# Kernel optimization log

Measured on AMD Instinct MI355X. Metric: run time of the kernel, lower is better.

Reference implementation:

```python
import jax, jax.numpy as jnp
import numpy as np

N_NODES = 10000
N_EDGES = 160000
C = 128           # channel multiplicity
D_DOWN = 64       # node_feats_down '64x0e'
D_RAD = 8         # radial basis size
AVG_NEIGH = 16.0
INV_SQRT3 = 1.0 / np.sqrt(3.0)  # CG coeff for 1o x 1o -> 0e


def setup_inputs() -> dict:
    key = jax.random.key(0)
    ks = jax.random.split(key, 20)
    inp = {
        "node_attrs": jax.random.normal(ks[0], (N_NODES, 10), jnp.float32),
        "node_feats": jax.random.normal(ks[1], (N_NODES, 4 * C), jnp.float32),
        "edge_attrs": jax.random.normal(ks[2], (N_EDGES, 4), jnp.float32),
        "edge_feats": jax.random.uniform(ks[3], (N_EDGES, D_RAD), jnp.float32),
        "edge_index": jax.random.randint(ks[4], (N_EDGES, 2), 0, N_NODES, jnp.int32),
        # linear_up: 128x0e+128x1o -> 128x0e+128x1o (per-irrep channel mixing)
        "W_up0": jax.random.normal(ks[5], (C, C), jnp.float32),
        "W_up1": jax.random.normal(ks[6], (C, C), jnp.float32),
        # linear_down: 128x0e+128x1o -> 64x0e (only scalars map)
        "W_down": jax.random.normal(ks[7], (C, D_DOWN), jnp.float32),
        # radial MLP [136, 256, 256, 256, 512]
        "Wm0": jax.random.normal(ks[8], (D_RAD + 2 * D_DOWN, 256), jnp.float32),
        "Wm1": jax.random.normal(ks[9], (256, 256), jnp.float32),
        "Wm2": jax.random.normal(ks[10], (256, 256), jnp.float32),
        "Wm3": jax.random.normal(ks[11], (256, 4 * C), jnp.float32),
        # linear: irreps_mid (2x128x0e + 2x128x1o) -> 128x0e+128x1o
        "W_lin0": jax.random.normal(ks[12], (2 * C, C), jnp.float32),
        "W_lin1": jax.random.normal(ks[13], (2 * C, C), jnp.float32),
        # skip_linear: 128x0e+128x1o -> 128x0e+128x1o
        "W_skip0": jax.random.normal(ks[14], (C, C), jnp.float32),
        "W_skip1": jax.random.normal(ks[15], (C, C), jnp.float32),
    }
    return inp


def _split(x):
    # [N, 512] -> scalars [N,128], vectors [N,128,3]
    return x[:, :C], x[:, C:].reshape(-1, C, 3)


def _irrep_linear(s, v, W0, W1):
    # e3nn Linear with 1/sqrt(fan_in) normalization, per-irrep
    a = (s @ W0) / np.sqrt(C)
    b = jnp.einsum("nic,ij->njc", v, W1) / np.sqrt(C)
    return a, b


def reference(node_attrs, node_feats, edge_attrs, edge_feats, edge_index,
              W_up0, W_up1, W_down, Wm0, Wm1, Wm2, Wm3,
              W_lin0, W_lin1, W_skip0, W_skip1):
    n_nodes = node_feats.shape[0]
    sender = edge_index[:, 0]
    receiver = edge_index[:, 1]

    s, v = _split(node_feats)

    # skip connection
    sc_s, sc_v = _irrep_linear(s, v, W_skip0, W_skip1)
    sc = jnp.concatenate([sc_s, sc_v.reshape(n_nodes, 3 * C)], axis=-1)

    # linear_up / linear_down
    up_s, up_v = _irrep_linear(s, v, W_up0, W_up1)
    down = (s @ W_down) / np.sqrt(C)  # [N, 64]

    # radial MLP on augmented edge feats
    aug = jnp.concatenate([edge_feats, down[sender], down[receiver]], axis=-1)  # [E,136]
    h = jax.nn.silu((aug @ Wm0) / np.sqrt(aug.shape[-1]))
    h = jax.nn.silu((h @ Wm1) / np.sqrt(256.0))
    h = jax.nn.silu((h @ Wm2) / np.sqrt(256.0))
    tpw = (h @ Wm3) / np.sqrt(256.0)  # [E, 512]
    w1, w2, w3, w4 = tpw[:, :C], tpw[:, C:2*C], tpw[:, 2*C:3*C], tpw[:, 3*C:]

    # per-edge CG tensor product (uvu, external weights)
    xs = up_s[sender]           # [E,128] gathered 0e
    xv = up_v[sender]           # [E,128,3] gathered 1o
    y0 = edge_attrs[:, :1]      # [E,1]   sh 0e
    yv = edge_attrs[:, 1:4]     # [E,3]   sh 1o

    out0a = w1 * xs * y0                                       # 0e x 0e -> 0e
    out0b = w4 * jnp.einsum("eic,ec->ei", xv, yv) * INV_SQRT3  # 1o x 1o -> 0e
    out1a = (w2 * xs)[:, :, None] * yv[:, None, :]             # 0e x 1o -> 1o
    out1b = w3[:, :, None] * xv * y0[:, :, None]               # 1o x 0e -> 1o

    mid0 = jnp.concatenate([out0a, out0b], axis=-1)  # [E,256]
    mid1 = jnp.concatenate([out1a, out1b], axis=1)   # [E,256,3]

    # scatter-sum messages to receivers
    m0 = jax.ops.segment_sum(mid0, receiver, num_segments=n_nodes)
    m1 = jax.ops.segment_sum(mid1, receiver, num_segments=n_nodes)

    # final per-irrep linear, divided by avg_num_neighbors
    msg_s = (m0 @ W_lin0) / np.sqrt(2.0 * C) / AVG_NEIGH                       # [N,128]
    msg_v = jnp.einsum("nic,ij->njc", m1, W_lin1) / np.sqrt(2.0 * C) / AVG_NEIGH  # [N,128,3]

    # reshape_irreps: [N, channels, 1+3]
    out = jnp.concatenate([msg_s[:, :, None], msg_v], axis=-1)  # [N,128,4]
    return out, sc
```

## Files before the change

### kernel.cpp

```cpp
#include <hip/hip_runtime.h>
#include <cmath>

#define NN 10000
#define NE 160000
#define INV_SQRT_C 0.08838834764831845f
#define INV_SQRT3F 0.5773502691896258f

typedef _Float16 f16x8 __attribute__((ext_vector_type(8)));
typedef _Float16 f16x4 __attribute__((ext_vector_type(4)));
typedef _Float16 f16x2 __attribute__((ext_vector_type(2)));
typedef float    f32x4 __attribute__((ext_vector_type(4)));

__device__ __forceinline__ float silu_f(float x) {
  return x / (1.f + __expf(-x));
}

__device__ __forceinline__ void wconv_one(
    int bx, const float* __restrict__ src, _Float16* __restrict__ dst,
    int Korig, int Kpad, int N, float scale, int P) {
  int total = Kpad * N;
  for (int t = bx * 256 + threadIdx.x; t < total; t += 128 * 256) {
    int n = t % N;
    int k = t / N;
    int kb = k >> 5, kk = k & 31;
    int sub = n & (P - 1);
    int n_l = (n & ~(P - 1)) | ((sub & 15) * (P >> 4) + (sub >> 4));
    float v = (k < Korig) ? src[(size_t)k * N + n_l] * scale : 0.f;
    dst[((size_t)(kb * N + n) << 5) + kk] = (_Float16)v;
  }
}

__device__ __forceinline__ void wconv_pair(
    int bx, const float* __restrict__ A, const float* __restrict__ B,
    _Float16* __restrict__ dst, float scale) {
  int tgl = bx * 256 + threadIdx.x;
  int n = tgl & 255;
  int k = tgl >> 8;
  int kb = k >> 5, kk = k & 31;
  int sub = n & 63;
  int n_l = (n & ~63) | ((sub & 15) * 4 + (sub >> 4));
  float v = ((n_l < 128) ? A[(size_t)k * 128 + n_l]
                         : B[(size_t)k * 128 + (n_l - 128)]) * scale;
  dst[((size_t)(kb * 256 + n) << 5) + kk] = (_Float16)v;
}

__device__ __forceinline__ void wconv_dn(
    int bx, const float* __restrict__ src, _Float16* __restrict__ dst,
    float scale) {
  int tgl = bx * 256 + threadIdx.x;
  int n = tgl & 63;
  int k = tgl >> 6;
  int kb = k >> 5, kk = k & 31;
  float v = src[(size_t)k * 64 + n] * scale;
  dst[((size_t)(kb * 64 + n) << 5) + kk] = (_Float16)v;
}

__global__ __launch_bounds__(256) void wconv9(
    const float* __restrict__ s0, const float* __restrict__ s1,
    const float* __restrict__ s2, const float* __restrict__ s3,
    const float* __restrict__ s4, const float* __restrict__ s5,
    _Float16* __restrict__ d0, _Float16* __restrict__ d1,
    _Float16* __restrict__ d2, _Float16* __restrict__ d3,
    _Float16* __restrict__ d4, _Float16* __restrict__ d5,
    const float* __restrict__ W_up0, const float* __restrict__ W_skip0,
    const float* __restrict__ W_up1, const float* __restrict__ W_skip1,
    const float* __restrict__ W_down,
    _Float16* __restrict__ WS0h, _Float16* __restrict__ WS1h,
    _Float16* __restrict__ WDh,
    const int* __restrict__ edge_index,
    int* __restrict__ CNT, int* __restrict__ CNT2) {
  const int b = blockIdx.x;
  if (b < 768) {
    const int job = b >> 7, bx = b & 127;
    switch (job) {
      case 0: wconv_one(bx, s0, d0, 136, 160, 256, 0.08574929257125442f, 64); break;
      case 1: wconv_one(bx, s1, d1, 256, 256, 256, 0.0625f, 64); break;
      case 2: wconv_one(bx, s2, d2, 256, 256, 256, 0.0625f, 64); break;
      case 3: wconv_one(bx, s3, d3, 256, 256, 512, 0.0625f, 32); break;
      case 4: wconv_one(bx, s4, d4, 256, 256, 128, 1.0f / 256.0f, 32); break;
      default: wconv_one(bx, s5, d5, 256, 256, 128, 1.0f / 256.0f, 32); break;
    }
  } else if (b < 896) {
    wconv_pair(b - 768, W_up0, W_skip0, WS0h, INV_SQRT_C);
  } else if (b < 1024) {
    wconv_pair(b - 896, W_up1, W_skip1, WS1h, INV_SQRT_C);
  } else if (b < 1056) {
    wconv_dn(b - 1024, W_down, WDh, INV_SQRT_C);
  } else {
    int e = (b - 1056) * 256 + threadIdx.x;
    if (e < NE) {
      int2 sr = *(const int2*)&edge_index[(size_t)e * 2];
      atomicAdd(&CNT[sr.y], 1);
      atomicAdd(&CNT2[sr.x], 1);
    }
  }
}

__global__ __launch_bounds__(256) void prep2(
    const float* __restrict__ feats,
    const _Float16* __restrict__ WS0h, const _Float16* __restrict__ WS1h,
    const _Float16* __restrict__ WDh,
    _Float16* __restrict__ UPH, _Float16* __restrict__ DOWNH,
    float* __restrict__ out_sc) {
  __shared__ _Float16 As[64 * 128];
  const int b = blockIdx.x;
  const int t = threadIdx.x;
  const int lane = t & 63;
  const int wv = t >> 6;
  const int m = lane & 15;
  const int g = lane >> 4;
  f32x4 zero4 = {0.f, 0.f, 0.f, 0.f};
  f16x8 zf = {0, 0, 0, 0, 0, 0, 0, 0};

  if (b < 157) {
    const int n0 = b * 64;
    for (int idx = t; idx < 1024; idx += 256) {
      int r = idx >> 4, c8 = idx & 15;
      int n = n0 + r;
      f16x8 av = zf;
      if (n < NN) {
        const float* src = &feats[(size_t)n * 512 + c8 * 8];
        float4 f0 = *(const float4*)src;
        float4 f1 = *(const float4*)(src + 4);
        av[0] = (_Float16)f0.x; av[1] = (_Float16)f0.y;
        av[2] = (_Float16)f0.z; av[3] = (_Float16)f0.w;
        av[4] = (_Float16)f1.x; av[5] = (_Float16)f1.y;
        av[6] = (_Float16)f1.z; av[7] = (_Float16)f1.w;
      }
      int sb = (c8 >> 1) ^ (r & 7);
      *(f16x8*)&As[r * 128 + (sb << 4) + (c8 & 1) * 8] = av;
    }
    __syncthreads();

    f32x4 acc[4][4];
    f32x4 acc2[4];
#pragma unroll
    for (int rt = 0; rt < 4; ++rt) {
      acc2[rt] = zero4;
#pragma unroll
      for (int ct = 0; ct < 4; ++ct) acc[rt][ct] = zero4;
    }
#pragma unroll
    for (int kb = 0; kb < 4; ++kb) {
      f16x8 a[4], bf[4];
#pragma unroll
      for (int rt = 0; rt < 4; ++rt) {
        int row = rt * 16 + m;
        a[rt] = *(const f16x8*)&As[row * 128 +
                 ((((kb * 2 + (g >> 1)) ^ (m & 7)) & 7) << 4) + (g & 1) * 8];
      }
#pragma unroll
      for (int ct = 0; ct < 4; ++ct)
        bf[ct] = *(const f16x8*)&WS0h[((size_t)(kb * 256 + wv * 64 + ct * 16 + m) << 5) + g * 8];
      f16x8 bd = *(const f16x8*)&WDh[((size_t)(kb * 64 + wv * 16 + m) << 5) + g * 8];
#pragma unroll
      for (int rt = 0; rt < 4; ++rt) {
#pragma unroll
        for (int ct = 0; ct < 4; ++ct)
          acc[rt][ct] = __builtin_amdgcn_mfma_f32_16x16x32_f16(a[rt], bf[ct], acc[rt][ct], 0, 0, 0);
        acc2[rt] = __builtin_amdgcn_mfma_f32_16x16x32_f16(a[rt], bd, acc2[rt], 0, 0, 0);
      }
    }
#pragma unroll
    for (int rt = 0; rt < 4; ++rt)
#pragma unroll
      for (int q = 0; q < 4; ++q) {
        int row = rt * 16 + g * 4 + q;
        int n = n0 + row;
        if (n >= NN) continue;
        if (wv < 2) {
          f16x4 pk;
#pragma unroll
          for (int ct = 0; ct < 4; ++ct) pk[ct] = (_Float16)acc[rt][ct][q];
          *(f16x4*)&UPH[(size_t)n * 512 + wv * 64 + m * 4] = pk;
        } else {
          float4 p4 = {acc[rt][0][q], acc[rt][1][q], acc[rt][2][q], acc[rt][3][q]};
          *(float4*)&out_sc[(size_t)n * 512 + (wv - 2) * 64 + m * 4] = p4;
        }
        DOWNH[(size_t)n * 64 + wv * 16 + m] = (_Float16)acc2[rt][q];
      }
  } else if (b < 626) {
    const int v0 = (b - 157) * 64;
    for (int idx = t; idx < 1024; idx += 256) {
      int r = idx >> 4, c8 = idx & 15;
      int rg = v0 + r;
      f16x8 av = zf;
      if (rg < 3 * NN) {
        int n = rg / 3, c = rg - n * 3;
        const float* src = &feats[(size_t)n * 512 + 128 + c];
#pragma unroll
        for (int z = 0; z < 8; ++z) av[z] = (_Float16)src[(c8 * 8 + z) * 3];
      }
      int sb = (c8 >> 1) ^ (r & 7);
      *(f16x8*)&As[r * 128 + (sb << 4) + (c8 & 1) * 8] = av;
    }
    __syncthreads();

    f32x4 acc[4][4];
#pragma unroll
    for (int rt = 0; rt < 4; ++rt)
#pragma unroll
      for (int ct = 0; ct < 4; ++ct) acc[rt][ct] = zero4;
#pragma unroll
    for (int kb = 0; kb < 4; ++kb) {
      f16x8 a[4], bf[4];
#pragma unroll
      for (int rt = 0; rt < 4; ++rt) {
        int row = rt * 16 + m;
        a[rt] = *(const f16x8*)&As[row * 128 +
                 ((((kb * 2 + (g >> 1)) ^ (m & 7)) & 7) << 4) + (g & 1) * 8];
      }
#pragma unroll
      for (int ct = 0; ct < 4; ++ct)
        bf[ct] = *(const f16x8*)&WS1h[((size_t)(kb * 256 + wv * 64 + ct * 16 + m) << 5) + g * 8];
#pragma unroll
      for (int rt = 0; rt < 4; ++rt)
#pragma unroll
        for (int ct = 0; ct < 4; ++ct)
          acc[rt][ct] = __builtin_amdgcn_mfma_f32_16x16x32_f16(a[rt], bf[ct], acc[rt][ct], 0, 0, 0);
    }
#pragma unroll
    for (int rt = 0; rt < 4; ++rt)
#pragma unroll
      for (int q = 0; q < 4; ++q) {
        int row = rt * 16 + g * 4 + q;
        int rg = v0 + row;
        if (rg >= 3 * NN) continue;
        int n = rg / 3, c = rg - (rg / 3) * 3;
        if (wv < 2) {
#pragma unroll
          for (int ct = 0; ct < 4; ++ct) {
            int j = wv * 64 + m * 4 + ct;
            UPH[(size_t)n * 512 + 128 + j * 3 + c] = (_Float16)acc[rt][ct][q];
          }
        } else {
#pragma unroll
          for (int ct = 0; ct < 4; ++ct) {
            int j = (wv - 2) * 64 + m * 4 + ct;
            out_sc[(size_t)n * 512 + 128 + j * 3 + c] = acc[rt][ct][q];
          }
        }
      }
  }
}

__device__ __forceinline__ void scan_one(const int* __restrict__ CNT,
                                         int* __restrict__ OFF,
                                         int* __restrict__ CUR, int* ts) {
  const int t = threadIdx.x;
  const int base = t * 10;
  int loc[10];
  int s = 0;
#pragma unroll
  for (int i = 0; i < 10; ++i) {
    int idx = base + i;
    int v = (idx < NN) ? CNT[idx] : 0;
    loc[i] = s;
    s += v;
  }
  ts[t] = s;
  __syncthreads();
  for (int off = 1; off < 1024; off <<= 1) {
    int v = (t >= off) ? ts[t - off] : 0;
    __syncthreads();
    ts[t] += v;
    __syncthreads();
  }
  int tp = (t > 0) ? ts[t - 1] : 0;
#pragma unroll
  for (int i = 0; i < 10; ++i) {
    int idx = base + i;
    if (idx < NN) {
      OFF[idx] = tp + loc[i];
      CUR[idx] = tp + loc[i];
    }
  }
  if (t == 1023) OFF[NN] = ts[1023];
}

__global__ __launch_bounds__(1024) void k_scan2(
    const int* __restrict__ CNT, int* __restrict__ OFF, int* __restrict__ CUR,
    const int* __restrict__ CNT2, int* __restrict__ OFF2, int* __restrict__ CUR2) {
  __shared__ int ts[1024];
  if (blockIdx.x == 0) scan_one(CNT, OFF, CUR, ts);
  else                 scan_one(CNT2, OFF2, CUR2, ts);
}

__global__ void k_fill2(const int* __restrict__ edge_index,
                        int* __restrict__ CUR, int* __restrict__ EIDX,
                        int* __restrict__ CUR2, int* __restrict__ SIDX) {
  int e = blockIdx.x * blockDim.x + threadIdx.x;
  if (e < NE) {
    int2 sr = *(const int2*)&edge_index[(size_t)e * 2];
    int ps = atomicAdd(&CUR2[sr.x], 1);
    SIDX[ps] = e;
    int pr = atomicAdd(&CUR[sr.y], 1);
    EIDX[pr] = ps;
  }
}

__device__ __forceinline__ void mlp_layer_256(
    const _Float16* In, _Float16* Out, const _Float16* __restrict__ Wz,
    int m, int g, int wv) {
  f32x4 acc[4][4];
  f32x4 zero4 = {0.f, 0.f, 0.f, 0.f};
#pragma unroll
  for (int rt = 0; rt < 4; ++rt)
#pragma unroll
    for (int ct = 0; ct < 4; ++ct) acc[rt][ct] = zero4;

#pragma unroll
  for (int kb = 0; kb < 8; ++kb) {
    f16x8 a[4], b[4];
#pragma unroll
    for (int rt = 0; rt < 4; ++rt) {
      int row = rt * 16 + m;
      a[rt] = *(const f16x8*)&In[row * 256 + (((kb * 2 + (g >> 1)) ^ m) << 4) + (g & 1) * 8];
    }
#pragma unroll
    for (int ct = 0; ct < 4; ++ct)
      b[ct] = *(const f16x8*)&Wz[((size_t)(kb * 256 + wv * 64 + ct * 16 + m) << 5) + g * 8];
#pragma unroll
    for (int rt = 0; rt < 4; ++rt)
#pragma unroll
      for (int ct = 0; ct < 4; ++ct)
        acc[rt][ct] = __builtin_amdgcn_mfma_f32_16x16x32_f16(a[rt], b[ct], acc[rt][ct], 0, 0, 0);
  }
#pragma unroll
  for (int rt = 0; rt < 4; ++rt)
#pragma unroll
    for (int q = 0; q < 4; ++q) {
      int row = rt * 16 + g * 4 + q;
      f16x4 pk;
#pragma unroll
      for (int ct = 0; ct < 4; ++ct) pk[ct] = (_Float16)silu_f(acc[rt][ct][q]);
      int blk = (wv * 4 + (m >> 2)) ^ (row & 15);
      *(f16x4*)&Out[row * 256 + (blk << 4) + (m & 3) * 4] = pk;
    }
}

__global__ __launch_bounds__(256, 2) void edge_mlp(
    const float* __restrict__ edge_attrs,
    const float* __restrict__ edge_feats,
    const int* __restrict__ edge_index,
    const int* __restrict__ SIDX,
    const _Float16* __restrict__ DOWNH,
    const _Float16* __restrict__ UPH,
    const _Float16* __restrict__ W0h, const _Float16* __restrict__ W1h,
    const _Float16* __restrict__ W2h, const _Float16* __restrict__ W3h,
    const _Float16* __restrict__ WL0h, const _Float16* __restrict__ WL1h,
    _Float16* __restrict__ MIDs) {
  __shared__ _Float16 HA[64 * 256];
  __shared__ _Float16 HB[64 * 256];
  __shared__ int    SNDs[64];
  __shared__ float4 EAs[64];

  const int tid = threadIdx.x;
  const int lane = tid & 63;
  const int wv = tid >> 6;
  const int m = lane & 15;
  const int g = lane >> 4;
  const int e0 = blockIdx.x * 64;
  const int nw = wv * 64;

  if (tid < 64) {
    int el = SIDX[e0 + tid];
    SNDs[tid] = edge_index[(size_t)el * 2];
    EAs[tid] = *(const float4*)&edge_attrs[(size_t)el * 4];
  }

  int el_r[4], snd_r[4], rcv_r[4];
#pragma unroll
  for (int rt = 0; rt < 4; ++rt) {
    el_r[rt] = SIDX[e0 + rt * 16 + m];
    int2 sr = *(const int2*)&edge_index[(size_t)el_r[rt] * 2];
    snd_r[rt] = sr.x;
    rcv_r[rt] = sr.y;
  }

  f32x4 zero4 = {0.f, 0.f, 0.f, 0.f};
  f16x8 zf = {0, 0, 0, 0, 0, 0, 0, 0};

  {
    f32x4 acc[4][4];
#pragma unroll
    for (int rt = 0; rt < 4; ++rt)
#pragma unroll
      for (int ct = 0; ct < 4; ++ct) acc[rt][ct] = zero4;

#pragma unroll
    for (int kb = 0; kb < 5; ++kb) {
      const int k0 = kb * 32 + g * 8;
      f16x8 a[4], b[4];
#pragma unroll
      for (int rt = 0; rt < 4; ++rt) {
        if (k0 == 0) {
          const float* ef = &edge_feats[(size_t)el_r[rt] * 8];
          float4 f0 = *(const float4*)ef;
          float4 f1 = *(const float4*)(ef + 4);
          f16x8 av;
          av[0] = (_Float16)f0.x; av[1] = (_Float16)f0.y;
          av[2] = (_Float16)f0.z; av[3] = (_Float16)f0.w;
          av[4] = (_Float16)f1.x; av[5] = (_Float16)f1.y;
          av[6] = (_Float16)f1.z; av[7] = (_Float16)f1.w;
          a[rt] = av;
        } else if (k0 < 72) {
          a[rt] = *(const f16x8*)&DOWNH[(size_t)snd_r[rt] * 64 + (k0 - 8)];
        } else if (k0 < 136) {
          a[rt] = *(const f16x8*)&DOWNH[(size_t)rcv_r[rt] * 64 + (k0 - 72)];
        } else {
          a[rt] = zf;
        }
      }
#pragma unroll
      for (int ct = 0; ct < 4; ++ct)
        b[ct] = *(const f16x8*)&W0h[((size_t)(kb * 256 + nw + ct * 16 + m) << 5) + g * 8];
#pragma unroll
      for (int rt = 0; rt < 4; ++rt)
#pragma unroll
        for (int ct = 0; ct < 4; ++ct)
          acc[rt][ct] = __builtin_amdgcn_mfma_f32_16x16x32_f16(a[rt], b[ct], acc[rt][ct], 0, 0, 0);
    }
#pragma unroll
    for (int rt = 0; rt < 4; ++rt)
#pragma unroll
      for (int q = 0; q < 4; ++q) {
        int row = rt * 16 + g * 4 + q;
        f16x4 pk;
#pragma unroll
        for (int ct = 0; ct < 4; ++ct) pk[ct] = (_Float16)silu_f(acc[rt][ct][q]);
        int blk = (wv * 4 + (m >> 2)) ^ (row & 15);
        *(f16x4*)&HA[row * 256 + (blk << 4) + (m & 3) * 4] = pk;
      }
  }
  __syncthreads();

  mlp_layer_256(HA, HB, W1h, m, g, wv);
  __syncthreads();
  mlp_layer_256(HB, HA, W2h, m, g, wv);
  __syncthreads();

  _Float16* SW = HB;
  _Float16* SP = HB + 64 * 128;

  const int e_loc = lane;
  const int ers = (e_loc ^ (e_loc >> 3)) & 7;
  const int snd_e = SNDs[e_loc];
  const _Float16* uprow = &UPH[(size_t)snd_e * 512];

  auto qgemm = [&](int qbase, f32x4 (&accq)[4][2]) {
#pragma unroll
    for (int rt = 0; rt < 4; ++rt)
#pragma unroll
      for (int ct = 0; ct < 2; ++ct) accq[rt][ct] = zero4;
#pragma unroll
    for (int kb = 0; kb < 8; ++kb) {
      f16x8 a[4], b[2];
#pragma unroll
      for (int rt = 0; rt < 4; ++rt) {
        int row = rt * 16 + m;
        a[rt] = *(const f16x8*)&HA[row * 256 + (((kb * 2 + (g >> 1)) ^ m) << 4) + (g & 1) * 8];
      }
#pragma unroll
      for (int ct = 0; ct < 2; ++ct)
        b[ct] = *(const f16x8*)&W3h[((size_t)(kb * 512 + qbase + wv * 32 + ct * 16 + m) << 5) + g * 8];
#pragma unroll
      for (int rt = 0; rt < 4; ++rt)
#pragma unroll
        for (int ct = 0; ct < 2; ++ct)
          accq[rt][ct] = __builtin_amdgcn_mfma_f32_16x16x32_f16(a[rt], b[ct], accq[rt][ct], 0, 0, 0);
    }
  };

  auto sw_write = [&](const f32x4 (&accq)[4][2]) {
#pragma unroll
    for (int rt = 0; rt < 4; ++rt)
#pragma unroll
      for (int r4 = 0; r4 < 4; ++r4) {
        int row = rt * 16 + g * 4 + r4;
        int rs = (row ^ (row >> 3)) & 7;
        f16x2 pk;
        pk[0] = (_Float16)accq[rt][0][r4];
        pk[1] = (_Float16)accq[rt][1][r4];
        int blk = ((wv * 2 + (m >> 3)) ^ rs) & 7;
        *(f16x2*)&SW[row * 128 + (blk << 4) + (m & 7) * 2] = pk;
      }
  };

  auto fold = [&](const _Float16* __restrict__ WLh, int qpart, f32x4 (&P)[4][2]) {
#pragma unroll
    for (int rt = 0; rt < 4; ++rt)
#pragma unroll
      for (int ct = 0; ct < 2; ++ct) P[rt][ct] = zero4;
#pragma unroll
    for (int kb = 0; kb < 4; ++kb) {
      f16x8 a[4], b[2];
#pragma unroll
      for (int rt = 0; rt < 4; ++rt) {
        int row = rt * 16 + m;
        int rs = (row ^ (row >> 3)) & 7;
        a[rt] = *(const f16x8*)&SP[row * 128 + ((((kb * 2 + (g >> 1)) ^ rs) & 7) << 4) + (g & 1) * 8];
      }
#pragma unroll
      for (int ct = 0; ct < 2; ++ct)
        b[ct] = *(const f16x8*)&WLh[((size_t)((qpart * 4 + kb) * 128 + wv * 32 + ct * 16 + m) << 5) + g * 8];
#pragma unroll
      for (int rt = 0; rt < 4; ++rt)
#pragma unroll
        for (int ct = 0; ct < 2; ++ct)
          P[rt][ct] = __builtin_amdgcn_mfma_f32_16x16x32_f16(a[rt], b[ct], P[rt][ct], 0, 0, 0);
    }
  };

  auto tp_xs = [&]() {
#pragma unroll
    for (int cch = 0; cch < 4; ++cch) {
      int ib = nw / 2 + cch * 8;
      int blk = ((ib >> 4) ^ ers) & 7;
      int off = e_loc * 128 + (blk << 4) + (ib & 15);
      f16x8 swv = *(const f16x8*)&SW[off];
      f16x8 upv = *(const f16x8*)&uprow[ib];
      f16x8 pr = swv * upv;
      *(f16x8*)&SP[off] = pr;
    }
  };

  _Float16 xvb[96];
  auto load_xv = [&]() {
#pragma unroll
    for (int u = 0; u < 12; ++u) {
      f16x8 t = *(const f16x8*)&uprow[128 + wv * 96 + u * 8];
#pragma unroll
      for (int z = 0; z < 8; ++z) xvb[u * 8 + z] = t[z];
    }
  };

  auto tp_w4 = [&]() {
    float4 ea = EAs[e_loc];
#pragma unroll
    for (int cch = 0; cch < 4; ++cch) {
      int ib = nw / 2 + cch * 8;
      int blk = ((ib >> 4) ^ ers) & 7;
      int off = e_loc * 128 + (blk << 4) + (ib & 15);
      f16x8 swv = *(const f16x8*)&SW[off];
      f16x8 outv;
#pragma unroll
      for (int z = 0; z < 8; ++z) {
        int k = cch * 8 + z;
        float d = (float)xvb[k * 3] * ea.y + (float)xvb[k * 3 + 1] * ea.z +
                  (float)xvb[k * 3 + 2] * ea.w;
        outv[z] = (_Float16)((float)swv[z] * d);
      }
      *(f16x8*)&SP[off] = outv;
    }
  };

  auto tp_w3 = [&](int c) {
#pragma unroll
    for (int cch = 0; cch < 4; ++cch) {
      int ib = nw / 2 + cch * 8;
      int blk = ((ib >> 4) ^ ers) & 7;
      int off = e_loc * 128 + (blk << 4) + (ib & 15);
      f16x8 swv = *(const f16x8*)&SW[off];
      f16x8 outv;
#pragma unroll
      for (int z = 0; z < 8; ++z) {
        int k = cch * 8 + z;
        outv[z] = swv[z] * xvb[k * 3 + c];
      }
      *(f16x8*)&SP[off] = outv;
    }
  };

  f32x4 accqA[4][2], accqB[4][2];
  f32x4 P1[4][2], P4[4][2], P2[4][2], P3[4][2];

  qgemm(0, accqA);
  sw_write(accqA);
  tp_xs();
  qgemm(384, accqB);
  __syncthreads();
  fold(WL0h, 0, P1);
  sw_write(accqB);
  load_xv();
  __syncthreads();
  tp_w4();
  qgemm(128, accqA);
  __syncthreads();
  fold(WL0h, 1, P4);
  sw_write(accqA);

#pragma unroll
  for (int rt = 0; rt < 4; ++rt)
#pragma unroll
    for (int r4 = 0; r4 < 4; ++r4) {
      int row = rt * 16 + g * 4 + r4;
      float4 ea = EAs[row];
      f16x2 pk;
      pk[0] = (_Float16)(ea.x * P1[rt][0][r4] + INV_SQRT3F * P4[rt][0][r4]);
      pk[1] = (_Float16)(ea.x * P1[rt][1][r4] + INV_SQRT3F * P4[rt][1][r4]);
      *(f16x2*)&MIDs[(size_t)(e0 + row) * 512 + wv * 32 + m * 2] = pk;
    }
  __syncthreads();
  tp_xs();
  qgemm(256, accqB);
  __syncthreads();
  fold(WL1h, 0, P2);
  sw_write(accqB);
  __syncthreads();

#pragma unroll
  for (int c = 0; c < 3; ++c) {
    tp_w3(c);
    __syncthreads();
    fold(WL1h, 1, P3);
#pragma unroll
    for (int rt = 0; rt < 4; ++rt)
#pragma unroll
      for (int r4 = 0; r4 < 4; ++r4) {
        int row = rt * 16 + g * 4 + r4;
        float4 ea = EAs[row];
        float yvc = (c == 0) ? ea.y : (c == 1) ? ea.z : ea.w;
        f16x2 pk;
        pk[0] = (_Float16)(yvc * P2[rt][0][r4] + ea.x * P3[rt][0][r4]);
        pk[1] = (_Float16)(yvc * P2[rt][1][r4] + ea.x * P3[rt][1][r4]);
        *(f16x2*)&MIDs[(size_t)(e0 + row) * 512 + 128 + c * 128 + wv * 32 + m * 2] = pk;
      }
    if (c < 2) __syncthreads();
  }
}

__global__ __launch_bounds__(256) void gather_msg(
    const _Float16* __restrict__ MIDs, const int* __restrict__ OFF,
    const int* __restrict__ EIDX, float* __restrict__ out) {
  __shared__ int eb[256];
  __shared__ float os[512];
  const int n = blockIdx.x;
  const int t = threadIdx.x;
  const int beg = OFF[n], end = OFF[n + 1];
  float a0 = 0.f, a1 = 0.f;
  for (int base = beg; base < end; base += 256) {
    int cnt = min(256, end - base);
    __syncthreads();
    if (t < cnt) eb[t] = EIDX[base + t];
    __syncthreads();
    int k = 0;
    for (; k + 4 <= cnt; k += 4) {
      int e0_ = eb[k], e1_ = eb[k + 1], e2_ = eb[k + 2], e3_ = eb[k + 3];
      f16x2 v0 = *(const f16x2*)&MIDs[(size_t)e0_ * 512 + t * 2];
      f16x2 v1 = *(const f16x2*)&MIDs[(size_t)e1_ * 512 + t * 2];
      f16x2 v2 = *(const f16x2*)&MIDs[(size_t)e2_ * 512 + t * 2];
      f16x2 v3 = *(const f16x2*)&MIDs[(size_t)e3_ * 512 + t * 2];
      a0 += (float)v0[0] + (float)v1[0] + (float)v2[0] + (float)v3[0];
      a1 += (float)v0[1] + (float)v1[1] + (float)v2[1] + (float)v3[1];
    }
    for (; k < cnt; ++k) {
      f16x2 v = *(const f16x2*)&MIDs[(size_t)eb[k] * 512 + t * 2];
      a0 += (float)v[0];
      a1 += (float)v[1];
    }
  }
#pragma unroll
  for (int u = 0; u < 2; ++u) {
    int x = t * 2 + u;
    float a = u ? a1 : a0;
    int dst;
    if (x < 128) {
      dst = x * 4;
    } else {
      int xm = x - 128;
      int c = xm >> 7, j = xm & 127;
      dst = j * 4 + 1 + c;
    }
    os[dst] = a;
  }
  __syncthreads();
  *(float2*)&out[(size_t)n * 512 + t * 2] = *(const float2*)&os[t * 2];
}

extern "C" void kernel_launch(void* const* d_in, const int* in_sizes, int n_in,
                              void* d_out, int out_size, void* d_ws, size_t ws_size,
                              hipStream_t stream) {
  const float* node_feats = (const float*)d_in[1];
  const float* edge_attrs = (const float*)d_in[2];
  const float* edge_feats = (const float*)d_in[3];
  const int*   edge_index = (const int*)d_in[4];
  const float* W_up0   = (const float*)d_in[5];
  const float* W_up1   = (const float*)d_in[6];
  const float* W_down  = (const float*)d_in[7];
  const float* Wm0     = (const float*)d_in[8];
  const float* Wm1     = (const float*)d_in[9];
  const float* Wm2     = (const float*)d_in[10];
  const float* Wm3     = (const float*)d_in[11];
  const float* W_lin0  = (const float*)d_in[12];
  const float* W_lin1  = (const float*)d_in[13];
  const float* W_skip0 = (const float*)d_in[14];
  const float* W_skip1 = (const float*)d_in[15];
  float* out = (float*)d_out;

  char* ws = (char*)d_ws;
  size_t off = 0;
  auto alloc = [&](size_t bytes) {
    void* p = ws + off;
    off = (off + bytes + 255) & ~(size_t)255;
    return p;
  };
  _Float16* UPH   = (_Float16*)alloc((size_t)NN * 512 * 2);
  _Float16* DOWNH = (_Float16*)alloc((size_t)NN * 64 * 2);
  _Float16* W0h   = (_Float16*)alloc(160 * 256 * 2);
  _Float16* W1h   = (_Float16*)alloc(256 * 256 * 2);
  _Float16* W2h   = (_Float16*)alloc(256 * 256 * 2);
  _Float16* W3h   = (_Float16*)alloc(256 * 512 * 2);
  _Float16* WL0h  = (_Float16*)alloc(256 * 128 * 2);
  _Float16* WL1h  = (_Float16*)alloc(256 * 128 * 2);
  int*      CNTS  = (int*)alloc((size_t)2 * NN * 4);
  int*      CNT   = CNTS;
  int*      CNT2  = CNTS + NN;
  int*      OFF   = (int*)alloc((size_t)(NN + 1) * 4);
  int*      CUR   = (int*)alloc((size_t)NN * 4);
  int*      EIDX  = (int*)alloc((size_t)NE * 4);
  int*      OFF2  = (int*)alloc((size_t)(NN + 1) * 4);
  int*      CUR2  = (int*)alloc((size_t)NN * 4);
  int*      SIDX  = (int*)alloc((size_t)NE * 4);
  _Float16* MIDs  = (_Float16*)alloc((size_t)NE * 512 * 2);
  _Float16* WS0h  = (_Float16*)alloc(128 * 256 * 2);
  _Float16* WS1h  = (_Float16*)alloc(128 * 256 * 2);
  _Float16* WDh   = (_Float16*)alloc(128 * 64 * 2);

  hipMemsetAsync(CNTS, 0, (size_t)2 * NN * 4, stream);

  wconv9<<<1681, 256, 0, stream>>>(Wm0, Wm1, Wm2, Wm3, W_lin0, W_lin1,
                                   W0h, W1h, W2h, W3h, WL0h, WL1h,
                                   W_up0, W_skip0, W_up1, W_skip1, W_down,
                                   WS0h, WS1h, WDh,
                                   edge_index, CNT, CNT2);

  prep2<<<626, 256, 0, stream>>>(node_feats, WS0h, WS1h, WDh,
                                 UPH, DOWNH, out + (size_t)NN * 512);

  k_scan2<<<2, 1024, 0, stream>>>(CNT, OFF, CUR, CNT2, OFF2, CUR2);
  k_fill2<<<625, 256, 0, stream>>>(edge_index, CUR, EIDX, CUR2, SIDX);

  edge_mlp<<<2500, 256, 0, stream>>>(edge_attrs, edge_feats, edge_index, SIDX,
                                     DOWNH, UPH, W0h, W1h, W2h, W3h, WL0h, WL1h,
                                     MIDs);
  gather_msg<<<NN, 256, 0, stream>>>(MIDs, OFF, EIDX, out);
}
```

Measured before the change: 430.3 us.

## Double edge_mlp waves per block and fold scan into prep kernel

edge_mlp now runs 512 threads (8 waves) per 64-edge block, so each wave owns half as many output columns. That halves accumulator and xvb register footprints and the launch bounds request higher occupancy. The separate scan kernel is removed and the two prefix scans run as extra 256-thread blocks inside prep2, saving a launch. Weight conversion layout parameters change to match the new per-wave column split. The risk is narrower f16 stores to MIDs and more per-wave overhead for fewer MFMAs each.

```diff
diff --git a/kernel.cpp b/kernel.cpp
--- a/kernel.cpp
+++ b/kernel.cpp
@@ -76,9 +76,9 @@
       case 0: wconv_one(bx, s0, d0, 136, 160, 256, 0.08574929257125442f, 64); break;
       case 1: wconv_one(bx, s1, d1, 256, 256, 256, 0.0625f, 64); break;
       case 2: wconv_one(bx, s2, d2, 256, 256, 256, 0.0625f, 64); break;
-      case 3: wconv_one(bx, s3, d3, 256, 256, 512, 0.0625f, 32); break;
-      case 4: wconv_one(bx, s4, d4, 256, 256, 128, 1.0f / 256.0f, 32); break;
-      default: wconv_one(bx, s5, d5, 256, 256, 128, 1.0f / 256.0f, 32); break;
+      case 3: wconv_one(bx, s3, d3, 256, 256, 512, 0.0625f, 16); break;
+      case 4: wconv_one(bx, s4, d4, 256, 256, 128, 1.0f / 256.0f, 16); break;
+      default: wconv_one(bx, s5, d5, 256, 256, 128, 1.0f / 256.0f, 16); break;
     }
   } else if (b < 896) {
     wconv_pair(b - 768, W_up0, W_skip0, WS0h, INV_SQRT_C);
@@ -96,13 +96,46 @@
   }
 }
 
+__device__ __forceinline__ void scan_one256(const int* __restrict__ C,
+                                            int* __restrict__ O,
+                                            int* __restrict__ U, int* ts) {
+  const int t = threadIdx.x;
+  const int base = t * 40;
+  int s = 0;
+  for (int i = 0; i < 40; ++i) {
+    int idx = base + i;
+    if (idx < NN) s += C[idx];
+  }
+  ts[t] = s;
+  __syncthreads();
+  for (int off = 1; off < 256; off <<= 1) {
+    int v = (t >= off) ? ts[t - off] : 0;
+    __syncthreads();
+    ts[t] += v;
+    __syncthreads();
+  }
+  int run = (t > 0) ? ts[t - 1] : 0;
+  for (int i = 0; i < 40; ++i) {
+    int idx = base + i;
+    if (idx < NN) {
+      O[idx] = run;
+      U[idx] = run;
+      run += C[idx];
+    }
+  }
+  if (t == 255) O[NN] = ts[255];
+}
+
 __global__ __launch_bounds__(256) void prep2(
     const float* __restrict__ feats,
     const _Float16* __restrict__ WS0h, const _Float16* __restrict__ WS1h,
     const _Float16* __restrict__ WDh,
     _Float16* __restrict__ UPH, _Float16* __restrict__ DOWNH,
-    float* __restrict__ out_sc) {
+    float* __restrict__ out_sc,
+    const int* __restrict__ CNT, int* __restrict__ OFF, int* __restrict__ CUR,
+    const int* __restrict__ CNT2, int* __restrict__ OFF2, int* __restrict__ CUR2) {
   __shared__ _Float16 As[64 * 128];
+  __shared__ int ts[256];
   const int b = blockIdx.x;
   const int t = threadIdx.x;
   const int lane = t & 63;
@@ -111,6 +144,9 @@
   const int g = lane >> 4;
   f32x4 zero4 = {0.f, 0.f, 0.f, 0.f};
   f16x8 zf = {0, 0, 0, 0, 0, 0, 0, 0};
+
+  if (b == 626) { scan_one256(CNT, OFF, CUR, ts); return; }
+  if (b == 627) { scan_one256(CNT2, OFF2, CUR2, ts); return; }
 
   if (b < 157) {
     const int n0 = b * 64;
@@ -244,48 +280,6 @@
   }
 }
 
-__device__ __forceinline__ void scan_one(const int* __restrict__ CNT,
-                                         int* __restrict__ OFF,
-                                         int* __restrict__ CUR, int* ts) {
-  const int t = threadIdx.x;
-  const int base = t * 10;
-  int loc[10];
-  int s = 0;
-#pragma unroll
-  for (int i = 0; i < 10; ++i) {
-    int idx = base + i;
-    int v = (idx < NN) ? CNT[idx] : 0;
-    loc[i] = s;
-    s += v;
-  }
-  ts[t] = s;
-  __syncthreads();
-  for (int off = 1; off < 1024; off <<= 1) {
-    int v = (t >= off) ? ts[t - off] : 0;
-    __syncthreads();
-    ts[t] += v;
-    __syncthreads();
-  }
-  int tp = (t > 0) ? ts[t - 1] : 0;
-#pragma unroll
-  for (int i = 0; i < 10; ++i) {
-    int idx = base + i;
-    if (idx < NN) {
-      OFF[idx] = tp + loc[i];
-      CUR[idx] = tp + loc[i];
-    }
-  }
-  if (t == 1023) OFF[NN] = ts[1023];
-}
-
-__global__ __launch_bounds__(1024) void k_scan2(
-    const int* __restrict__ CNT, int* __restrict__ OFF, int* __restrict__ CUR,
-    const int* __restrict__ CNT2, int* __restrict__ OFF2, int* __restrict__ CUR2) {
-  __shared__ int ts[1024];
-  if (blockIdx.x == 0) scan_one(CNT, OFF, CUR, ts);
-  else                 scan_one(CNT2, OFF2, CUR2, ts);
-}
-
 __global__ void k_fill2(const int* __restrict__ edge_index,
                         int* __restrict__ CUR, int* __restrict__ EIDX,
                         int* __restrict__ CUR2, int* __restrict__ SIDX) {
@@ -299,31 +293,31 @@
   }
 }
 
-__device__ __forceinline__ void mlp_layer_256(
+__device__ __forceinline__ void mlp_layer_512(
     const _Float16* In, _Float16* Out, const _Float16* __restrict__ Wz,
     int m, int g, int wv) {
-  f32x4 acc[4][4];
+  f32x4 acc[4][2];
   f32x4 zero4 = {0.f, 0.f, 0.f, 0.f};
 #pragma unroll
   for (int rt = 0; rt < 4; ++rt)
 #pragma unroll
-    for (int ct = 0; ct < 4; ++ct) acc[rt][ct] = zero4;
+    for (int ct = 0; ct < 2; ++ct) acc[rt][ct] = zero4;
 
 #pragma unroll
   for (int kb = 0; kb < 8; ++kb) {
-    f16x8 a[4], b[4];
+    f16x8 a[4], b[2];
 #pragma unroll
     for (int rt = 0; rt < 4; ++rt) {
       int row = rt * 16 + m;
       a[rt] = *(const f16x8*)&In[row * 256 + (((kb * 2 + (g >> 1)) ^ m) << 4) + (g & 1) * 8];
     }
 #pragma unroll
-    for (int ct = 0; ct < 4; ++ct)
-      b[ct] = *(const f16x8*)&Wz[((size_t)(kb * 256 + wv * 64 + ct * 16 + m) << 5) + g * 8];
+    for (int ct = 0; ct < 2; ++ct)
+      b[ct] = *(const f16x8*)&Wz[((size_t)(kb * 256 + wv * 32 + ct * 16 + m) << 5) + g * 8];
 #pragma unroll
     for (int rt = 0; rt < 4; ++rt)
 #pragma unroll
-      for (int ct = 0; ct < 4; ++ct)
+      for (int ct = 0; ct < 2; ++ct)
         acc[rt][ct] = __builtin_amdgcn_mfma_f32_16x16x32_f16(a[rt], b[ct], acc[rt][ct], 0, 0, 0);
   }
 #pragma unroll
@@ -331,15 +325,15 @@
 #pragma unroll
     for (int q = 0; q < 4; ++q) {
       int row = rt * 16 + g * 4 + q;
-      f16x4 pk;
-#pragma unroll
-      for (int ct = 0; ct < 4; ++ct) pk[ct] = (_Float16)silu_f(acc[rt][ct][q]);
-      int blk = (wv * 4 + (m >> 2)) ^ (row & 15);
-      *(f16x4*)&Out[row * 256 + (blk << 4) + (m & 3) * 4] = pk;
-    }
-}
-
-__global__ __launch_bounds__(256, 2) void edge_mlp(
+      f16x2 pk;
+      pk[0] = (_Float16)silu_f(acc[rt][0][q]);
+      pk[1] = (_Float16)silu_f(acc[rt][1][q]);
+      int blk = ((wv >> 1) * 4 + (m >> 2)) ^ (row & 15);
+      *(f16x2*)&Out[row * 256 + (blk << 4) + (m & 3) * 4 + (wv & 1) * 2] = pk;
+    }
+}
+
+__global__ __launch_bounds__(512, 4) void edge_mlp(
     const float* __restrict__ edge_attrs,
     const float* __restrict__ edge_feats,
     const int* __restrict__ edge_index,
@@ -361,7 +355,6 @@
   const int m = lane & 15;
   const int g = lane >> 4;
   const int e0 = blockIdx.x * 64;
-  const int nw = wv * 64;
 
   if (tid < 64) {
     int el = SIDX[e0 + tid];
@@ -382,16 +375,16 @@
   f16x8 zf = {0, 0, 0, 0, 0, 0, 0, 0};
 
   {
-    f32x4 acc[4][4];
+    f32x4 acc[4][2];
 #pragma unroll
     for (int rt = 0; rt < 4; ++rt)
 #pragma unroll
-      for (int ct = 0; ct < 4; ++ct) acc[rt][ct] = zero4;
+      for (int ct = 0; ct < 2; ++ct) acc[rt][ct] = zero4;
 
 #pragma unroll
     for (int kb = 0; kb < 5; ++kb) {
       const int k0 = kb * 32 + g * 8;
-      f16x8 a[4], b[4];
+      f16x8 a[4], b[2];
 #pragma unroll
       for (int rt = 0; rt < 4; ++rt) {
         if (k0 == 0) {
@@ -413,12 +406,12 @@
         }
       }
 #pragma unroll
-      for (int ct = 0; ct < 4; ++ct)
-        b[ct] = *(const f16x8*)&W0h[((size_t)(kb * 256 + nw + ct * 16 + m) << 5) + g * 8];
+      for (int ct = 0; ct < 2; ++ct)
+        b[ct] = *(const f16x8*)&W0h[((size_t)(kb * 256 + wv * 32 + ct * 16 + m) << 5) + g * 8];
 #pragma unroll
       for (int rt = 0; rt < 4; ++rt)
 #pragma unroll
-        for (int ct = 0; ct < 4; ++ct)
+        for (int ct = 0; ct < 2; ++ct)
           acc[rt][ct] = __builtin_amdgcn_mfma_f32_16x16x32_f16(a[rt], b[ct], acc[rt][ct], 0, 0, 0);
     }
 #pragma unroll
@@ -426,18 +419,18 @@
 #pragma unroll
       for (int q = 0; q < 4; ++q) {
         int row = rt * 16 + g * 4 + q;
-        f16x4 pk;
-#pragma unroll
-        for (int ct = 0; ct < 4; ++ct) pk[ct] = (_Float16)silu_f(acc[rt][ct][q]);
-        int blk = (wv * 4 + (m >> 2)) ^ (row & 15);
-        *(f16x4*)&HA[row * 256 + (blk << 4) + (m & 3) * 4] = pk;
-      }
-  }
-  __syncthreads();
-
-  mlp_layer_256(HA, HB, W1h, m, g, wv);
-  __syncthreads();
-  mlp_layer_256(HB, HA, W2h, m, g, wv);
+        f16x2 pk;
+        pk[0] = (_Float16)silu_f(acc[rt][0][q]);
+        pk[1] = (_Float16)silu_f(acc[rt][1][q]);
+        int blk = ((wv >> 1) * 4 + (m >> 2)) ^ (row & 15);
+        *(f16x2*)&HA[row * 256 + (blk << 4) + (m & 3) * 4 + (wv & 1) * 2] = pk;
+      }
+  }
+  __syncthreads();
+
+  mlp_layer_512(HA, HB, W1h, m, g, wv);
+  __syncthreads();
+  mlp_layer_512(HB, HA, W2h, m, g, wv);
   __syncthreads();
 
   _Float16* SW = HB;
@@ -448,74 +441,59 @@
   const int snd_e = SNDs[e_loc];
   const _Float16* uprow = &UPH[(size_t)snd_e * 512];
 
-  auto qgemm = [&](int qbase, f32x4 (&accq)[4][2]) {
-#pragma unroll
-    for (int rt = 0; rt < 4; ++rt)
-#pragma unroll
-      for (int ct = 0; ct < 2; ++ct) accq[rt][ct] = zero4;
+  auto qgemm = [&](int qbase, f32x4 (&accq)[4]) {
+#pragma unroll
+    for (int rt = 0; rt < 4; ++rt) accq[rt] = zero4;
 #pragma unroll
     for (int kb = 0; kb < 8; ++kb) {
-      f16x8 a[4], b[2];
+      f16x8 a[4], b;
 #pragma unroll
       for (int rt = 0; rt < 4; ++rt) {
         int row = rt * 16 + m;
         a[rt] = *(const f16x8*)&HA[row * 256 + (((kb * 2 + (g >> 1)) ^ m) << 4) + (g & 1) * 8];
       }
-#pragma unroll
-      for (int ct = 0; ct < 2; ++ct)
-        b[ct] = *(const f16x8*)&W3h[((size_t)(kb * 512 + qbase + wv * 32 + ct * 16 + m) << 5) + g * 8];
+      b = *(const f16x8*)&W3h[((size_t)(kb * 512 + qbase + wv * 16 + m) << 5) + g * 8];
 #pragma unroll
       for (int rt = 0; rt < 4; ++rt)
-#pragma unroll
-        for (int ct = 0; ct < 2; ++ct)
-          accq[rt][ct] = __builtin_amdgcn_mfma_f32_16x16x32_f16(a[rt], b[ct], accq[rt][ct], 0, 0, 0);
+        accq[rt] = __builtin_amdgcn_mfma_f32_16x16x32_f16(a[rt], b, accq[rt], 0, 0, 0);
     }
   };
 
-  auto sw_write = [&](const f32x4 (&accq)[4][2]) {
+  auto sw_write = [&](const f32x4 (&accq)[4]) {
 #pragma unroll
     for (int rt = 0; rt < 4; ++rt)
 #pragma unroll
       for (int r4 = 0; r4 < 4; ++r4) {
         int row = rt * 16 + g * 4 + r4;
         int rs = (row ^ (row >> 3)) & 7;
-        f16x2 pk;
-        pk[0] = (_Float16)accq[rt][0][r4];
-        pk[1] = (_Float16)accq[rt][1][r4];
-        int blk = ((wv * 2 + (m >> 3)) ^ rs) & 7;
-        *(f16x2*)&SW[row * 128 + (blk << 4) + (m & 7) * 2] = pk;
+        int blk = (wv ^ rs) & 7;
+        SW[row * 128 + (blk << 4) + m] = (_Float16)accq[rt][r4];
       }
   };
 
-  auto fold = [&](const _Float16* __restrict__ WLh, int qpart, f32x4 (&P)[4][2]) {
-#pragma unroll
-    for (int rt = 0; rt < 4; ++rt)
-#pragma unroll
-      for (int ct = 0; ct < 2; ++ct) P[rt][ct] = zero4;
+  auto fold = [&](const _Float16* __restrict__ WLh, int qpart, f32x4 (&P)[4]) {
+#pragma unroll
+    for (int rt = 0; rt < 4; ++rt) P[rt] = zero4;
 #pragma unroll
     for (int kb = 0; kb < 4; ++kb) {
-      f16x8 a[4], b[2];
+      f16x8 a[4], b;
 #pragma unroll
       for (int rt = 0; rt < 4; ++rt) {
         int row = rt * 16 + m;
         int rs = (row ^ (row >> 3)) & 7;
         a[rt] = *(const f16x8*)&SP[row * 128 + ((((kb * 2 + (g >> 1)) ^ rs) & 7) << 4) + (g & 1) * 8];
       }
-#pragma unroll
-      for (int ct = 0; ct < 2; ++ct)
-        b[ct] = *(const f16x8*)&WLh[((size_t)((qpart * 4 + kb) * 128 + wv * 32 + ct * 16 + m) << 5) + g * 8];
+      b = *(const f16x8*)&WLh[((size_t)((qpart * 4 + kb) * 128 + wv * 16 + m) << 5) + g * 8];
 #pragma unroll
       for (int rt = 0; rt < 4; ++rt)
-#pragma unroll
-        for (int ct = 0; ct < 2; ++ct)
-          P[rt][ct] = __builtin_amdgcn_mfma_f32_16x16x32_f16(a[rt], b[ct], P[rt][ct], 0, 0, 0);
+        P[rt] = __builtin_amdgcn_mfma_f32_16x16x32_f16(a[rt], b, P[rt], 0, 0, 0);
     }
   };
 
   auto tp_xs = [&]() {
 #pragma unroll
-    for (int cch = 0; cch < 4; ++cch) {
-      int ib = nw / 2 + cch * 8;
+    for (int cch = 0; cch < 2; ++cch) {
+      int ib = wv * 16 + cch * 8;
       int blk = ((ib >> 4) ^ ers) & 7;
       int off = e_loc * 128 + (blk << 4) + (ib & 15);
       f16x8 swv = *(const f16x8*)&SW[off];
@@ -525,11 +503,11 @@
     }
   };
 
-  _Float16 xvb[96];
+  _Float16 xvb[48];
   auto load_xv = [&]() {
 #pragma unroll
-    for (int u = 0; u < 12; ++u) {
-      f16x8 t = *(const f16x8*)&uprow[128 + wv * 96 + u * 8];
+    for (int u = 0; u < 6; ++u) {
+      f16x8 t = *(const f16x8*)&uprow[128 + wv * 48 + u * 8];
 #pragma unroll
       for (int z = 0; z < 8; ++z) xvb[u * 8 + z] = t[z];
     }
@@ -538,8 +516,8 @@
   auto tp_w4 = [&]() {
     float4 ea = EAs[e_loc];
 #pragma unroll
-    for (int cch = 0; cch < 4; ++cch) {
-      int ib = nw / 2 + cch * 8;
+    for (int cch = 0; cch < 2; ++cch) {
+      int ib = wv * 16 + cch * 8;
       int blk = ((ib >> 4) ^ ers) & 7;
       int off = e_loc * 128 + (blk << 4) + (ib & 15);
       f16x8 swv = *(const f16x8*)&SW[off];
@@ -557,8 +535,8 @@
 
   auto tp_w3 = [&](int c) {
 #pragma unroll
-    for (int cch = 0; cch < 4; ++cch) {
-      int ib = nw / 2 + cch * 8;
+    for (int cch = 0; cch < 2; ++cch) {
+      int ib = wv * 16 + cch * 8;
       int blk = ((ib >> 4) ^ ers) & 7;
       int off = e_loc * 128 + (blk << 4) + (ib & 15);
       f16x8 swv = *(const f16x8*)&SW[off];
@@ -572,8 +550,9 @@
     }
   };
 
-  f32x4 accqA[4][2], accqB[4][2];
-  f32x4 P1[4][2], P4[4][2], P2[4][2], P3[4][2];
+  f32x4 accqA[4], accqB[4];
+  f32x4 P1[4], P4[4], P2[4], P3[4];
+  const int co = wv * 16 + m;
 
   qgemm(0, accqA);
   sw_write(accqA);
@@ -596,10 +575,8 @@
     for (int r4 = 0; r4 < 4; ++r4) {
       int row = rt * 16 + g * 4 + r4;
       float4 ea = EAs[row];
-      f16x2 pk;
-      pk[0] = (_Float16)(ea.x * P1[rt][0][r4] + INV_SQRT3F * P4[rt][0][r4]);
-      pk[1] = (_Float16)(ea.x * P1[rt][1][r4] + INV_SQRT3F * P4[rt][1][r4]);
-      *(f16x2*)&MIDs[(size_t)(e0 + row) * 512 + wv * 32 + m * 2] = pk;
+      MIDs[(size_t)(e0 + row) * 512 + co] =
+          (_Float16)(ea.x * P1[rt][r4] + INV_SQRT3F * P4[rt][r4]);
     }
   __syncthreads();
   tp_xs();
@@ -621,10 +598,8 @@
         int row = rt * 16 + g * 4 + r4;
         float4 ea = EAs[row];
         float yvc = (c == 0) ? ea.y : (c == 1) ? ea.z : ea.w;
-        f16x2 pk;
-        pk[0] = (_Float16)(yvc * P2[rt][0][r4] + ea.x * P3[rt][0][r4]);
-        pk[1] = (_Float16)(yvc * P2[rt][1][r4] + ea.x * P3[rt][1][r4]);
-        *(f16x2*)&MIDs[(size_t)(e0 + row) * 512 + 128 + c * 128 + wv * 32 + m * 2] = pk;
+        MIDs[(size_t)(e0 + row) * 512 + 128 + c * 128 + co] =
+            (_Float16)(yvc * P2[rt][r4] + ea.x * P3[rt][r4]);
       }
     if (c < 2) __syncthreads();
   }
@@ -735,13 +710,13 @@
                                    WS0h, WS1h, WDh,
                                    edge_index, CNT, CNT2);
 
-  prep2<<<626, 256, 0, stream>>>(node_feats, WS0h, WS1h, WDh,
-                                 UPH, DOWNH, out + (size_t)NN * 512);
-
-  k_scan2<<<2, 1024, 0, stream>>>(CNT, OFF, CUR, CNT2, OFF2, CUR2);
+  prep2<<<628, 256, 0, stream>>>(node_feats, WS0h, WS1h, WDh,
+                                 UPH, DOWNH, out + (size_t)NN * 512,
+                                 CNT, OFF, CUR, CNT2, OFF2, CUR2);
+
   k_fill2<<<625, 256, 0, stream>>>(edge_index, CUR, EIDX, CUR2, SIDX);
 
-  edge_mlp<<<2500, 256, 0, stream>>>(edge_attrs, edge_feats, edge_index, SIDX,
+  edge_mlp<<<2500, 512, 0, stream>>>(edge_attrs, edge_feats, edge_index, SIDX,
                                      DOWNH, UPH, W0h, W1h, W2h, W3h, WL0h, WL1h,
                                      MIDs);
   gather_msg<<<NN, 256, 0, stream>>>(MIDs, OFF, EIDX, out);
```

Measured after the change: 548.9 us. 1.28x slower.
